# Performance work log

Hardware: AMD Instinct MI355X
Metric: run time of the kernel (lower is better)

The kernel has to match this reference:

```python
import jax, jax.numpy as jnp
import numpy as np

B, D, E, T = 262144, 128, 8, 3   # batch, input_dim, num_experts, num_tasks
H1, H2, G = 64, 32, 64           # expert hidden dims, gate hidden dim


def setup_inputs() -> dict:
    key = jax.random.key(0)
    ks = jax.random.split(key, 9)
    s = 0.05
    return {
        "x":   jax.random.normal(ks[0], (B, D), dtype=jnp.float32),
        # stacked expert MLP params: D -> H1 (relu) -> H2 (relu)
        "We1": jax.random.normal(ks[1], (E, D, H1), dtype=jnp.float32) * s,
        "be1": jax.random.normal(ks[2], (E, H1), dtype=jnp.float32) * s,
        "We2": jax.random.normal(ks[3], (E, H1, H2), dtype=jnp.float32) * s,
        "be2": jax.random.normal(ks[4], (E, H2), dtype=jnp.float32) * s,
        # stacked gate MLP params: D -> G (relu) -> E (linear, then softmax)
        "Wg1": jax.random.normal(ks[5], (T, D, G), dtype=jnp.float32) * s,
        "bg1": jax.random.normal(ks[6], (T, G), dtype=jnp.float32) * s,
        "Wg2": jax.random.normal(ks[7], (T, G, E), dtype=jnp.float32) * s,
        "bg2": jax.random.normal(ks[8], (T, E), dtype=jnp.float32) * s,
    }


def reference(x, We1, be1, We2, be2, Wg1, bg1, Wg2, bg2):
    # All experts as one batched GEMM chain: [B,E,H1] -> [B,E,H2]
    h1 = jax.nn.relu(jnp.einsum('bd,edh->beh', x, We1) + be1)
    experts_out = jax.nn.relu(jnp.einsum('beh,eho->beo', h1, We2) + be2)  # [B,E,H2]
    # All task gates as one batched GEMM chain: [B,T,E]
    g = jax.nn.relu(jnp.einsum('bd,tdh->bth', x, Wg1) + bg1)
    gate = jax.nn.softmax(jnp.einsum('bth,the->bte', g, Wg2) + bg2, axis=-1)
    # softmax-weighted sum over experts, per task
    out = jnp.einsum('bte,beo->bto', gate, experts_out)  # [B,T,H2]
    return tuple(out[:, t] for t in range(T))
```

## Files before the change

### kernel.cpp

```cpp
#include <hip/hip_runtime.h>

#define BROWS 262144
#define OUT_TASK_F32 8388608

#define WS_L1F 0
#define WS_L2F 196608
#define WS_B1  235520
#define WS_B2  238592

#define H1B 0
#define EOB 49152
#define SGB 81920
#define XSB 84992
#define LDS_TOTAL 101376

typedef __attribute__((ext_vector_type(8))) short bf16x8;
typedef __attribute__((ext_vector_type(4))) float f32x4;
typedef __attribute__((ext_vector_type(2))) unsigned int u32x2;
typedef __attribute__((ext_vector_type(4))) unsigned int u32x4;

#define MFMA16(a, b, c) __builtin_amdgcn_mfma_f32_16x16x32_bf16((a), (b), (c), 0, 0, 0)

__device__ __forceinline__ unsigned short f2bf(float f) {
  unsigned int u = __float_as_uint(f);
  return (unsigned short)((u + 0x7FFFu + ((u >> 16) & 1u)) >> 16);
}
__device__ __forceinline__ unsigned int cvtpk(float lo, float hi) {
  unsigned int r;
  asm("v_cvt_pk_bf16_f32 %0, %1, %2" : "=v"(r) : "v"(lo), "v"(hi));
  return r;
}

__global__ void pack_kernel(const float* __restrict__ We1, const float* __restrict__ be1,
                            const float* __restrict__ We2, const float* __restrict__ be2,
                            const float* __restrict__ Wg1, const float* __restrict__ bg1,
                            const float* __restrict__ Wg2, const float* __restrict__ bg2,
                            unsigned char* __restrict__ ws) {
  int idx = blockIdx.x * blockDim.x + threadIdx.x;
  unsigned short* L1F = (unsigned short*)(ws + WS_L1F);
  unsigned short* L2F = (unsigned short*)(ws + WS_L2F);
  float* B1 = (float*)(ws + WS_B1);
  float* B2 = (float*)(ws + WS_B2);
  if (idx < 98304) {
    int j = idx & 7, lane = (idx >> 3) & 63, ks = (idx >> 9) & 3, nt = idx >> 11;
    int k = ks * 32 + ((lane >> 4) << 3) + j;
    int n = nt * 16 + (lane & 15);
    float v = 0.f;
    if (n < 512)      v = We1[((n >> 6) * 128 + k) * 64 + (n & 63)];
    else if (n < 704) v = Wg1[(((n - 512) >> 6) * 128 + k) * 64 + ((n - 512) & 63)];
    L1F[idx] = f2bf(v);
  } else if (idx < 98304 + 19456) {
    int i2 = idx - 98304;
    int j = i2 & 7, lane = (i2 >> 3) & 63, ks = (i2 >> 9) & 1, nt = i2 >> 10;
    int k = ks * 32 + ((lane >> 4) << 3) + j;
    int n = nt * 16 + (lane & 15);
    float v = 0.f;
    if (n < 256) v = We2[((n >> 5) * 64 + k) * 32 + (n & 31)];
    else { int g = n - 256, t = g >> 4, eo = g & 15; if (eo < 8) v = Wg2[(t * 64 + k) * 8 + eo]; }
    L2F[i2] = f2bf(v);
  } else if (idx < 98304 + 19456 + 768) {
    int n = idx - (98304 + 19456);
    float v = 0.f;
    if (n < 512)      v = be1[n];
    else if (n < 704) v = bg1[n - 512];
    B1[n] = v;
  } else if (idx < 98304 + 19456 + 768 + 304) {
    int n = idx - (98304 + 19456 + 768);
    float v = 0.f;
    if (n < 256) v = be2[n];
    else { int g = n - 256, t = g >> 4, eo = g & 15; if (eo < 8) v = bg2[t * 8 + eo]; }
    B2[n] = v;
  }
}

__global__ __launch_bounds__(512, 2) void mmoe_kernel(const float* __restrict__ x,
                                                      const unsigned char* __restrict__ ws,
                                                      float* __restrict__ out) {
  __shared__ unsigned char lds[LDS_TOTAL];

  const int tid = threadIdx.x;
  const int l   = tid & 63;
  const int wid = tid >> 6;
  const int l15 = l & 15;
  const int lhi = l >> 4;
  const int swz = (l15 & 7) << 4;

  const bf16x8* L1F = (const bf16x8*)(ws + WS_L1F);
  const bf16x8* L2F = (const bf16x8*)(ws + WS_L2F);
  const float*  B1  = (const float*)(ws + WS_B1);
  const float*  B2  = (const float*)(ws + WS_B2);

  int ntb[6];
#pragma unroll
  for (int i = 0; i < 6; ++i) ntb[i] = wid * 6 + i;
  if (wid >= 6) {
    int b = wid - 6;
#pragma unroll
    for (int i = 0; i < 4; ++i) ntb[i] = 36 + b * 4 + i;
    ntb[4] = 44 + b * 2; ntb[5] = 45 + b * 2;
  }

  bf16x8 w1f[6][4];
  f32x4 b1v[6];
#pragma unroll
  for (int i = 0; i < 6; ++i) {
#pragma unroll
    for (int ks = 0; ks < 4; ++ks) w1f[i][ks] = L1F[(ntb[i] * 4 + ks) * 64 + l];
    b1v[i] = *(const f32x4*)(B1 + ntb[i] * 16 + lhi * 4);
  }
  bf16x8 w2f[2][2];
  f32x4 b2v[2];
#pragma unroll
  for (int i = 0; i < 2; ++i) {
#pragma unroll
    for (int ks = 0; ks < 2; ++ks) w2f[i][ks] = L2F[((wid * 2 + i) * 2 + ks) * 64 + l];
    b2v[i] = *(const f32x4*)(B2 + wid * 32 + i * 16 + lhi * 4);
  }
  bf16x8 wgf[2];
  f32x4 bgv = (f32x4){0.f, 0.f, 0.f, 0.f};
  if (wid >= 5) {
    int t = wid - 5;
#pragma unroll
    for (int ks = 0; ks < 2; ++ks) wgf[ks] = L2F[((16 + t) * 2 + ks) * 64 + l];
    bgv = *(const f32x4*)(B2 + 256 + t * 16 + lhi * 4);
  }

  const int r32 = tid >> 4;
  const int c8  = (tid & 15) * 8;
  const int sboff = (r32 >> 4) * 4096 + (r32 & 15) * 256 + (((tid & 15) * 16) ^ ((r32 & 7) << 4));
  const int rowbase = blockIdx.x * 1024;

  {
    const float* xp = x + (size_t)(rowbase + r32) * 128 + c8;
    float4 a = *(const float4*)xp, b = *(const float4*)(xp + 4);
    u32x4 p; p[0] = cvtpk(a.x, a.y); p[1] = cvtpk(a.z, a.w);
    p[2] = cvtpk(b.x, b.y); p[3] = cvtpk(b.z, b.w);
    *(u32x4*)(lds + XSB + sboff) = p;
  }
  __syncthreads();

  int cur = 0;
#pragma unroll 1
  for (int it = 0; it < 32; ++it) {
    float4 sa, sb;
    const bool stage = (it + 1 < 32);
    if (stage) {
      const float* xp = x + (size_t)(rowbase + (it + 1) * 32 + r32) * 128 + c8;
      sa = *(const float4*)xp; sb = *(const float4*)(xp + 4);
    }

    if (it > 0 && wid < 4) {
      const int m = wid >> 1;
      const int c = lhi + 4 * (wid & 1);
      const unsigned char* sgp = lds + SGB + m * 1536 + l15 * 96;
      f32x4 g0a = *(const f32x4*)(sgp +  0), g0b = *(const f32x4*)(sgp + 16);
      f32x4 g1a = *(const f32x4*)(sgp + 32), g1b = *(const f32x4*)(sgp + 48);
      f32x4 g2a = *(const f32x4*)(sgp + 64), g2b = *(const f32x4*)(sgp + 80);
      f32x4 v0 = (f32x4){0.f,0.f,0.f,0.f}, v1 = v0, v2 = v0;
#pragma unroll
      for (int e = 0; e < 8; ++e) {
        f32x4 eo = *(const f32x4*)(lds + EOB + m * 16384 + l15 * 1024 +
                                   ((e * 128 + c * 16) ^ swz));
        float ga = (e < 4) ? g0a[e & 3] : g0b[e & 3];
        float gb = (e < 4) ? g1a[e & 3] : g1b[e & 3];
        float gc = (e < 4) ? g2a[e & 3] : g2b[e & 3];
        v0 += ga * eo; v1 += gb * eo; v2 += gc * eo;
      }
      size_t rowg = (size_t)(rowbase + (it - 1) * 32 + m * 16 + l15) * 32 + c * 4;
      *(float4*)(out + rowg)                    = (float4){v0[0], v0[1], v0[2], v0[3]};
      *(float4*)(out + OUT_TASK_F32 + rowg)     = (float4){v1[0], v1[1], v1[2], v1[3]};
      *(float4*)(out + 2 * OUT_TASK_F32 + rowg) = (float4){v2[0], v2[1], v2[2], v2[3]};
    }

#pragma unroll
    for (int m = 0; m < 2; ++m) {
      bf16x8 xa[4];
#pragma unroll
      for (int ks = 0; ks < 4; ++ks)
        xa[ks] = *(const bf16x8*)(lds + XSB + cur * 8192 + m * 4096 + l15 * 256 +
                                  ((ks * 64 + lhi * 16) ^ swz));
      f32x4 acc[6];
#pragma unroll
      for (int i = 0; i < 6; ++i) acc[i] = b1v[i];
#pragma unroll
      for (int ks = 0; ks < 4; ++ks)
#pragma unroll
        for (int i = 0; i < 6; ++i)
          acc[i] = MFMA16(w1f[i][ks], xa[ks], acc[i]);
#pragma unroll
      for (int i = 0; i < 6; ++i) {
        u32x2 p;
        p[0] = cvtpk(fmaxf(acc[i][0], 0.f), fmaxf(acc[i][1], 0.f));
        p[1] = cvtpk(fmaxf(acc[i][2], 0.f), fmaxf(acc[i][3], 0.f));
        *(u32x2*)(lds + H1B + m * 24576 + l15 * 1536 + ((ntb[i] * 32 + lhi * 8) ^ swz)) = p;
      }
    }
    __syncthreads();

#pragma unroll
    for (int m = 0; m < 2; ++m) {
      bf16x8 hb0 = *(const bf16x8*)(lds + H1B + m * 24576 + l15 * 1536 + ((wid * 128 + lhi * 16) ^ swz));
      bf16x8 hb1 = *(const bf16x8*)(lds + H1B + m * 24576 + l15 * 1536 + ((wid * 128 + 64 + lhi * 16) ^ swz));
      f32x4 a2[2] = {b2v[0], b2v[1]};
#pragma unroll
      for (int i = 0; i < 2; ++i) {
        a2[i] = MFMA16(w2f[i][0], hb0, a2[i]);
        a2[i] = MFMA16(w2f[i][1], hb1, a2[i]);
        f32x4 r;
        r[0] = fmaxf(a2[i][0], 0.f); r[1] = fmaxf(a2[i][1], 0.f);
        r[2] = fmaxf(a2[i][2], 0.f); r[3] = fmaxf(a2[i][3], 0.f);
        *(f32x4*)(lds + EOB + m * 16384 + l15 * 1024 + ((wid * 128 + i * 64 + lhi * 16) ^ swz)) = r;
      }

      if (wid >= 5) {
        int t = wid - 5;
        bf16x8 gb0 = *(const bf16x8*)(lds + H1B + m * 24576 + l15 * 1536 + ((1024 + t * 128 + lhi * 16) ^ swz));
        bf16x8 gb1 = *(const bf16x8*)(lds + H1B + m * 24576 + l15 * 1536 + ((1024 + t * 128 + 64 + lhi * 16) ^ swz));
        f32x4 ag = bgv;
        ag = MFMA16(wgf[0], gb0, ag);
        ag = MFMA16(wgf[1], gb1, ag);
        float s0 = ag[0], s1 = ag[1], s2 = ag[2], s3 = ag[3];
        float o0 = __shfl_xor(s0, 16), o1 = __shfl_xor(s1, 16);
        float o2 = __shfl_xor(s2, 16), o3 = __shfl_xor(s3, 16);
        float mx = fmaxf(fmaxf(fmaxf(s0, s1), fmaxf(s2, s3)),
                         fmaxf(fmaxf(o0, o1), fmaxf(o2, o3)));
        float q0 = __expf(s0 - mx), q1 = __expf(s1 - mx), q2 = __expf(s2 - mx), q3 = __expf(s3 - mx);
        float ps = q0 + q1 + q2 + q3;
        float inv = 1.f / (ps + __shfl_xor(ps, 16));
        if (lhi < 2)
          *(f32x4*)(lds + SGB + m * 1536 + l15 * 96 + t * 32 + lhi * 16) =
              (f32x4){q0 * inv, q1 * inv, q2 * inv, q3 * inv};
      }
    }

    if (stage) {
      u32x4 p; p[0] = cvtpk(sa.x, sa.y); p[1] = cvtpk(sa.z, sa.w);
      p[2] = cvtpk(sb.x, sb.y); p[3] = cvtpk(sb.z, sb.w);
      *(u32x4*)(lds + XSB + (cur ^ 1) * 8192 + sboff) = p;
    }
    __syncthreads();
    cur ^= 1;
  }

  if (wid < 4) {
    const int m = wid >> 1;
    const int c = lhi + 4 * (wid & 1);
    const unsigned char* sgp = lds + SGB + m * 1536 + l15 * 96;
    f32x4 g0a = *(const f32x4*)(sgp +  0), g0b = *(const f32x4*)(sgp + 16);
    f32x4 g1a = *(const f32x4*)(sgp + 32), g1b = *(const f32x4*)(sgp + 48);
    f32x4 g2a = *(const f32x4*)(sgp + 64), g2b = *(const f32x4*)(sgp + 80);
    f32x4 v0 = (f32x4){0.f,0.f,0.f,0.f}, v1 = v0, v2 = v0;
#pragma unroll
    for (int e = 0; e < 8; ++e) {
      f32x4 eo = *(const f32x4*)(lds + EOB + m * 16384 + l15 * 1024 +
                                 ((e * 128 + c * 16) ^ swz));
      float ga = (e < 4) ? g0a[e & 3] : g0b[e & 3];
      float gb = (e < 4) ? g1a[e & 3] : g1b[e & 3];
      float gc = (e < 4) ? g2a[e & 3] : g2b[e & 3];
      v0 += ga * eo; v1 += gb * eo; v2 += gc * eo;
    }
    size_t rowg = (size_t)(rowbase + 31 * 32 + m * 16 + l15) * 32 + c * 4;
    *(float4*)(out + rowg)                    = (float4){v0[0], v0[1], v0[2], v0[3]};
    *(float4*)(out + OUT_TASK_F32 + rowg)     = (float4){v1[0], v1[1], v1[2], v1[3]};
    *(float4*)(out + 2 * OUT_TASK_F32 + rowg) = (float4){v2[0], v2[1], v2[2], v2[3]};
  }
}

extern "C" void kernel_launch(void* const* d_in, const int* in_sizes, int n_in,
                              void* d_out, int out_size, void* d_ws, size_t ws_size,
                              hipStream_t stream) {
  const float* x   = (const float*)d_in[0];
  const float* We1 = (const float*)d_in[1];
  const float* be1 = (const float*)d_in[2];
  const float* We2 = (const float*)d_in[3];
  const float* be2 = (const float*)d_in[4];
  const float* Wg1 = (const float*)d_in[5];
  const float* bg1 = (const float*)d_in[6];
  const float* Wg2 = (const float*)d_in[7];
  const float* bg2 = (const float*)d_in[8];
  unsigned char* ws = (unsigned char*)d_ws;
  float* out = (float*)d_out;

  pack_kernel<<<465, 256, 0, stream>>>(We1, be1, We2, be2, Wg1, bg1, Wg2, bg2, ws);
  mmoe_kernel<<<256, 512, 0, stream>>>(x, ws, out);
}
```

Baseline: 92.28 us.

## Load x fragments directly into registers instead of staging through LDS

Removes the LDS staging buffer for the input tile. Each wave now prefetches its own MFMA operand fragments of x from global memory into registers one iteration ahead and converts them to bf16 in place. This cuts LDS traffic and usage, but every compute wave now reads the full x tile redundantly from global/L2 memory. It also holds a large register prefetch buffer, which may reduce occupancy.

```diff
diff --git a/kernel.cpp b/kernel.cpp
--- a/kernel.cpp
+++ b/kernel.cpp
@@ -11,8 +11,7 @@
 #define H1B 0
 #define EOB 49152
 #define SGB 81920
-#define XSB 84992
-#define LDS_TOTAL 101376
+#define LDS_TOTAL 84992
 
 typedef __attribute__((ext_vector_type(8))) short bf16x8;
 typedef __attribute__((ext_vector_type(4))) float f32x4;
@@ -125,29 +124,23 @@
     bgv = *(const f32x4*)(B2 + 256 + t * 16 + lhi * 4);
   }
 
-  const int r32 = tid >> 4;
-  const int c8  = (tid & 15) * 8;
-  const int sboff = (r32 >> 4) * 4096 + (r32 & 15) * 256 + (((tid & 15) * 16) ^ ((r32 & 7) << 4));
   const int rowbase = blockIdx.x * 1024;
 
-  {
-    const float* xp = x + (size_t)(rowbase + r32) * 128 + c8;
-    float4 a = *(const float4*)xp, b = *(const float4*)(xp + 4);
-    u32x4 p; p[0] = cvtpk(a.x, a.y); p[1] = cvtpk(a.z, a.w);
-    p[2] = cvtpk(b.x, b.y); p[3] = cvtpk(b.z, b.w);
-    *(u32x4*)(lds + XSB + sboff) = p;
-  }
-  __syncthreads();
-
-  int cur = 0;
+  float4 nx[2][8];
+#pragma unroll
+  for (int m = 0; m < 2; ++m) {
+    const float* xp = x + (size_t)(rowbase + m * 16 + l15) * 128 + lhi * 8;
+#pragma unroll
+    for (int ks = 0; ks < 4; ++ks) {
+      nx[m][2 * ks]     = *(const float4*)(xp + ks * 32);
+      nx[m][2 * ks + 1] = *(const float4*)(xp + ks * 32 + 4);
+    }
+  }
+
+  int dummy = 0; (void)dummy;
 #pragma unroll 1
   for (int it = 0; it < 32; ++it) {
-    float4 sa, sb;
     const bool stage = (it + 1 < 32);
-    if (stage) {
-      const float* xp = x + (size_t)(rowbase + (it + 1) * 32 + r32) * 128 + c8;
-      sa = *(const float4*)xp; sb = *(const float4*)(xp + 4);
-    }
 
     if (it > 0 && wid < 4) {
       const int m = wid >> 1;
@@ -176,9 +169,21 @@
     for (int m = 0; m < 2; ++m) {
       bf16x8 xa[4];
 #pragma unroll
-      for (int ks = 0; ks < 4; ++ks)
-        xa[ks] = *(const bf16x8*)(lds + XSB + cur * 8192 + m * 4096 + l15 * 256 +
-                                  ((ks * 64 + lhi * 16) ^ swz));
+      for (int ks = 0; ks < 4; ++ks) {
+        float4 a = nx[m][2 * ks], b = nx[m][2 * ks + 1];
+        u32x4 u;
+        u[0] = cvtpk(a.x, a.y); u[1] = cvtpk(a.z, a.w);
+        u[2] = cvtpk(b.x, b.y); u[3] = cvtpk(b.z, b.w);
+        xa[ks] = *(bf16x8*)&u;
+      }
+      if (stage) {
+        const float* xp = x + (size_t)(rowbase + (it + 1) * 32 + m * 16 + l15) * 128 + lhi * 8;
+#pragma unroll
+        for (int ks = 0; ks < 4; ++ks) {
+          nx[m][2 * ks]     = *(const float4*)(xp + ks * 32);
+          nx[m][2 * ks + 1] = *(const float4*)(xp + ks * 32 + 4);
+        }
+      }
       f32x4 acc[6];
 #pragma unroll
       for (int i = 0; i < 6; ++i) acc[i] = b1v[i];
@@ -232,14 +237,7 @@
               (f32x4){q0 * inv, q1 * inv, q2 * inv, q3 * inv};
       }
     }
-
-    if (stage) {
-      u32x4 p; p[0] = cvtpk(sa.x, sa.y); p[1] = cvtpk(sa.z, sa.w);
-      p[2] = cvtpk(sb.x, sb.y); p[3] = cvtpk(sb.z, sb.w);
-      *(u32x4*)(lds + XSB + (cur ^ 1) * 8192 + sboff) = p;
-    }
     __syncthreads();
-    cur ^= 1;
   }
 
   if (wid < 4) {
```

Measured after the change: 291.2 us. +215.6%, slower.
